# Kernel tuning notes

Measured on AMD Instinct MI355X. Metric: run time of the kernel, lower is better.

Reference implementation:

```python
import jax, jax.numpy as jnp
import numpy as np

E = 1024   # embed_dim
H = 16     # num_heads
D = E // H # head_dim
BS = 512   # block_size
G = 128    # global_len
B = 1
S = 8192


def setup_inputs() -> dict:
    key = jax.random.key(0)
    ks = jax.random.split(key, 7)
    w_scale = 0.02
    return {
        "token_hidden_states": jax.random.normal(ks[0], (B, S, E), jnp.float32),
        "global_hidden_states": jax.random.normal(ks[1], (B, G, E), jnp.float32),
        "attention_mask": jnp.zeros((B, S), jnp.float32),  # additive float mask
        "Wq": jax.random.normal(ks[2], (E, E), jnp.float32) * w_scale,
        "Wk": jax.random.normal(ks[3], (E, E), jnp.float32) * w_scale,
        "Wv": jax.random.normal(ks[4], (E, E), jnp.float32) * w_scale,
        "Wo": jax.random.normal(ks[5], (E, E), jnp.float32) * w_scale,
    }


def _shape(x):
    # [B, L, E] -> [B, H, L, D]
    b, l, _ = x.shape
    return x.reshape(b, l, H, D).transpose(0, 2, 1, 3)


def reference(token_hidden_states, global_hidden_states, attention_mask, Wq, Wk, Wv, Wo):
    b, s, _ = token_hidden_states.shape
    g = global_hidden_states.shape[1]
    n = s // BS  # num_blocks
    scaling = D ** -0.5

    local_q = _shape(token_hidden_states @ Wq * scaling)
    local_k = _shape(token_hidden_states @ Wk)
    local_v = _shape(token_hidden_states @ Wv)
    global_q = _shape(global_hidden_states @ Wq * scaling)
    global_k = _shape(global_hidden_states @ Wk)
    global_v = _shape(global_hidden_states @ Wv)

    # ---- global attention: global queries attend to [global + all local] keys
    k_cat = jnp.concatenate([global_k, local_k], axis=2)   # [B,H,G+S,D]
    v_cat = jnp.concatenate([global_v, local_v], axis=2)
    ext_mask = jnp.pad(attention_mask, ((0, 0), (g, 0)))    # [B,G+S]
    gw = jnp.einsum('bhgf,bhxf->bhgx', global_q, k_cat) + ext_mask[:, None, None, :]
    gp = jax.nn.softmax(gw, axis=-1)
    g_out = jnp.einsum('bhgx,bhxf->bhgf', gp, v_cat)        # [B,H,G,D]
    g_out = g_out.transpose(0, 2, 1, 3).reshape(b, g, E) @ Wo

    # ---- local attention: block-local + global keys
    bq = local_q.reshape(b, H, n, BS, D)
    bk = local_k.reshape(b, H, n, BS, D)
    bv = local_v.reshape(b, H, n, BS, D)
    ext_mask_l = jnp.pad(attention_mask.reshape(b, n, BS), ((0, 0), (0, 0), (g, 0)))  # [B,N,G+K]
    l2g = jnp.einsum('bhnkf,bhgf->bhnkg', bq, global_k)     # [B,H,N,K,G]
    l2l = jnp.einsum('bhnkf,bhnxf->bhnkx', bq, bk)          # [B,H,N,K,K]
    lw = jnp.concatenate([l2g, l2l], axis=-1) + ext_mask_l[:, None, :, None, :]
    lp = jax.nn.softmax(lw, axis=-1)
    l_out = (jnp.einsum('bhnkg,bhgf->bhnkf', lp[..., :g], global_v)
             + jnp.einsum('bhnkx,bhnxf->bhnkf', lp[..., g:], bv))  # [B,H,N,K,D]
    l_out = l_out.transpose(0, 2, 3, 1, 4).reshape(b, s, E) @ Wo

    return (l_out, g_out)
```

## Files before the change

### kernel.cpp

```cpp
#include <hip/hip_runtime.h>
#include <stdint.h>

#define S_LEN  8192
#define G_LEN  128
#define E_DIM  1024
#define H_NUM  16
#define BS_LEN 512
#define R_TOT  8320
#define KBLK   128
#define XBLK   1040
#define NSPL   10
#define SPLW   832

typedef _Float16 half8    __attribute__((ext_vector_type(8)));
typedef _Float16 half4    __attribute__((ext_vector_type(4)));
typedef float    floatx4  __attribute__((ext_vector_type(4)));
typedef float    floatx16 __attribute__((ext_vector_type(16)));

#define QSCALE 0.18033688011112042f

#define OFF_XP   0
#define OFF_AOP  0
#define OFF_WP   17039360
#define SZ_WP1   2097152
#define OFF_QP   25427968
#define OFF_KP   42467328
#define OFF_VP   59506688
#define OFF_FH   76546048
#define OFF_OG   76579328
#define OFF_LG   81822208

__device__ __forceinline__ floatx16 zero16() {
  floatx16 v;
#pragma unroll
  for (int i = 0; i < 16; ++i) v[i] = 0.0f;
  return v;
}
__device__ __forceinline__ floatx4 zero4() {
  floatx4 v;
#pragma unroll
  for (int i = 0; i < 4; ++i) v[i] = 0.0f;
  return v;
}

__device__ __forceinline__ void gl_lds16(const void* g, void* l) {
  __builtin_amdgcn_global_load_lds(
      (const __attribute__((address_space(1))) void*)g,
      (__attribute__((address_space(3))) void*)l, 16, 0, 0);
}

__device__ __forceinline__ int pk_f16x2(float a, float b) {
  return __builtin_bit_cast(int, __builtin_amdgcn_cvt_pkrtz(a, b));
}

__global__ __launch_bounds__(256) void prep_k(const float* __restrict__ tok,
                                              const float* __restrict__ glob,
                                              const float* __restrict__ Wq,
                                              const float* __restrict__ Wk,
                                              const float* __restrict__ Wv,
                                              const float* __restrict__ Wo,
                                              const float* __restrict__ mask,
                                              char* __restrict__ ws) {
  __shared__ __align__(16) _Float16 tile[64 * 132];
  const int bx  = blockIdx.x;
  const int tid = threadIdx.x;
  if (bx < 1040) {
    const int r0 = (bx >> 3) * 64;
    const int c0 = (bx & 7) * 128;
#pragma unroll
    for (int kk = 0; kk < 8; ++kk) {
      int f   = tid + kk * 256;
      int row = f >> 5;
      int c4  = (f & 31) * 4;
      int r   = r0 + row;
      const float* src = (r < G_LEN) ? glob + (size_t)r * E_DIM
                                     : tok + (size_t)(r - G_LEN) * E_DIM;
      float4 v = *(const float4*)&src[c0 + c4];
      half4 h;
      h[0] = (_Float16)v.x; h[1] = (_Float16)v.y; h[2] = (_Float16)v.z; h[3] = (_Float16)v.w;
      *(half4*)&tile[row * 132 + c4] = h;
    }
    __syncthreads();
    _Float16* Xp = (_Float16*)(ws + OFF_XP);
#pragma unroll
    for (int uu = 0; uu < 4; ++uu) {
      int u    = tid + uu * 256;
      int kb_l = u >> 6;
      int row  = u & 63;
      half4 a = *(const half4*)&tile[row * 132 + kb_l * 8];
      half4 b = *(const half4*)&tile[row * 132 + kb_l * 8 + 4];
      half8 o;
      o[0] = a[0]; o[1] = a[1]; o[2] = a[2]; o[3] = a[3];
      o[4] = b[0]; o[5] = b[1]; o[6] = b[2]; o[7] = b[3];
      int kb = (c0 >> 3) + kb_l;
      *(half8*)&Xp[((size_t)kb * R_TOT + r0 + row) * 8] = o;
    }
  } else {
    int t = (bx - 1040) * 256 + tid;
    const int NW = 4 * KBLK * 1024;
    if (t < NW) {
      int w   = t >> 17;
      int rem = t & 131071;
      int kb  = rem >> 10;
      int n   = rem & 1023;
      const float* W = (w == 0) ? Wq : (w == 1) ? Wk : (w == 2) ? Wv : Wo;
      half8 v;
#pragma unroll
      for (int j = 0; j < 8; ++j)
        v[j] = (_Float16)W[(size_t)(kb * 8 + j) * 1024 + n];
      *(half8*)(ws + OFF_WP + (size_t)w * SZ_WP1 + (size_t)(kb * 1024 + n) * 16) = v;
    } else {
      int t2 = t - NW;
      if (t2 < R_TOT) {
        _Float16* fh = (_Float16*)(ws + OFF_FH);
        float m = (t2 < G_LEN) ? 0.0f : mask[t2 - G_LEN];
        fh[t2] = (_Float16)__expf(m);
      }
    }
  }
}

__device__ __forceinline__ void gemm_tile(const _Float16* __restrict__ Ap,
                                          const _Float16* __restrict__ Bp,
                                          int m0, int n0, _Float16* lds,
                                          floatx4 acc[4][4]) {
  const int tid  = threadIdx.x;
  const int wave = tid >> 6;
  const int lane = tid & 63;
  const int quad = lane >> 4;
  const int l16  = lane & 15;
  _Float16* As = lds;
  _Float16* Bs = lds + 8 * 128 * 8;
  const int wm = (wave >> 1) * 64;
  const int wn = (wave & 1) * 64;
  for (int step = 0; step < 16; ++step) {
#pragma unroll
    for (int ui = 0; ui < 8; ++ui) {
      const int u   = wave * 8 + ui;
      const int isB = u >> 4;
      const int vv  = u & 15;
      const int kb  = vv >> 1;
      const int rh  = vv & 1;
      const _Float16* src =
          isB ? Bp + (size_t)((step * 8 + kb) * 1024 + n0 + rh * 64 + lane) * 8
              : Ap + (size_t)((step * 8 + kb) * R_TOT + m0 + rh * 64 + lane) * 8;
      _Float16* dst = (isB ? Bs : As) + (kb * 128 + rh * 64) * 8;
      gl_lds16(src, dst);
    }
    __syncthreads();
#pragma unroll
    for (int kk = 0; kk < 2; ++kk) {
      half8 af[4], bf[4];
#pragma unroll
      for (int mt = 0; mt < 4; ++mt)
        af[mt] = *(const half8*)(As + ((kk * 4 + quad) * 128 + wm + mt * 16 + l16) * 8);
#pragma unroll
      for (int nt = 0; nt < 4; ++nt)
        bf[nt] = *(const half8*)(Bs + ((kk * 4 + quad) * 128 + wn + nt * 16 + l16) * 8);
#pragma unroll
      for (int mt = 0; mt < 4; ++mt)
#pragma unroll
        for (int nt = 0; nt < 4; ++nt)
          acc[mt][nt] = __builtin_amdgcn_mfma_f32_16x16x32_f16(bf[nt], af[mt], acc[mt][nt], 0, 0, 0);
    }
    __syncthreads();
  }
}

__global__ __launch_bounds__(256) void qkv_gemm_k(char* __restrict__ ws) {
  __shared__ __align__(16) _Float16 lds[2 * 8 * 128 * 8];
  const int z  = blockIdx.x >> 3;
  const int n0 = (blockIdx.x & 7) * 128;
  const int m0 = blockIdx.y * 128;
  floatx4 acc[4][4];
#pragma unroll
  for (int a = 0; a < 4; ++a)
#pragma unroll
    for (int b = 0; b < 4; ++b) acc[a][b] = zero4();
  gemm_tile((const _Float16*)(ws + OFF_XP),
            (const _Float16*)(ws + OFF_WP + (size_t)z * SZ_WP1), m0, n0, lds, acc);

  const int lane = threadIdx.x & 63, wave = threadIdx.x >> 6;
  const int quad = lane >> 4, l16 = lane & 15;
  const int wm = (wave >> 1) * 64, wn = (wave & 1) * 64;
  if (z < 2) {
    _Float16* dst = (_Float16*)(ws + (z == 0 ? OFF_QP : OFF_KP));
    const float scale = (z == 0) ? QSCALE : 1.0f;
#pragma unroll
    for (int mt = 0; mt < 4; ++mt)
#pragma unroll
      for (int nt = 0; nt < 4; ++nt) {
        int m  = m0 + wm + mt * 16 + l16;
        int nb = n0 + wn + nt * 16 + quad * 4;
        half4 h;
#pragma unroll
        for (int r = 0; r < 4; ++r) h[r] = (_Float16)(acc[mt][nt][r] * scale);
        int db = (nb >> 6) * 8 + ((nb & 63) >> 3);
        *(half4*)&dst[((size_t)db * R_TOT + m) * 8 + (nb & 7)] = h;
      }
  } else {
    _Float16* dst = (_Float16*)(ws + OFF_VP);
    const _Float16* fh = (const _Float16*)(ws + OFF_FH);
#pragma unroll
    for (int mt = 0; mt < 4; ++mt) {
      int m = m0 + wm + mt * 16 + l16;
      float fhm = (float)fh[m];
#pragma unroll
      for (int nt = 0; nt < 4; ++nt) {
        int nl = n0 + wn + nt * 16 + quad * 4;
#pragma unroll
        for (int r = 0; r < 4; ++r) {
          int n = nl + r;
          dst[(((size_t)(n >> 6) * XBLK + (m >> 3)) * 64 + (n & 63)) * 8 + (m & 7)] =
              (_Float16)(acc[mt][nt][r] * fhm);
        }
      }
    }
  }
}

__device__ __forceinline__ void attn_chunks(const _Float16* __restrict__ Kph,
                                            const _Float16* __restrict__ Vph,
                                            const _Float16* __restrict__ fh,
                                            const half8 qa[4], int lane,
                                            int kbase0, int nch,
                                            floatx16& o0, floatx16& o1, floatx16& lacc) {
  const int  half_ = lane >> 5;
  const int  c     = lane & 31;
  const bool hb    = half_ != 0;
  half8 kf[4];
#pragma unroll
  for (int ks = 0; ks < 4; ++ks)
    kf[ks] = *(const half8*)&Kph[(size_t)((ks * 2 + half_) * R_TOT + kbase0 + c) * 8];
  for (int ci = 0; ci < nch; ++ci) {
    const int kb = kbase0 + ci * 32;
    const int xb = kb >> 3;
    half8 vA0 = *(const half8*)&Vph[(size_t)((xb + half_) * 64 + c) * 8];
    half8 vA1 = *(const half8*)&Vph[(size_t)((xb + 2 + half_) * 64 + c) * 8];
    half8 vB0 = *(const half8*)&Vph[(size_t)((xb + half_) * 64 + 32 + c) * 8];
    half8 vB1 = *(const half8*)&Vph[(size_t)((xb + 2 + half_) * 64 + 32 + c) * 8];
    half8 f0 = *(const half8*)&fh[kb + half_ * 8];
    half8 f1 = *(const half8*)&fh[kb + 16 + half_ * 8];
    floatx16 s = zero16();
#pragma unroll
    for (int ks = 0; ks < 4; ++ks)
      s = __builtin_amdgcn_mfma_f32_32x32x16_f16(kf[ks], qa[ks], s, 0, 0, 0);
    const int kbn = (ci + 1 < nch) ? kb + 32 : kbase0;
#pragma unroll
    for (int ks = 0; ks < 4; ++ks)
      kf[ks] = *(const half8*)&Kph[(size_t)((ks * 2 + half_) * R_TOT + kbn + c) * 8];
    int pk[8];
#pragma unroll
    for (int i = 0; i < 8; ++i) {
      float e0 = __builtin_amdgcn_exp2f(s[2 * i]);
      float e1 = __builtin_amdgcn_exp2f(s[2 * i + 1]);
      pk[i] = pk_f16x2(e0, e1);
    }
    int sw[8];
#pragma unroll
    for (int i = 0; i < 8; ++i) sw[i] = __shfl_xor(pk[i], 32);
    int4 bi0, bi1;
    bi0.x = hb ? sw[2] : pk[0];  bi0.y = hb ? sw[3] : pk[1];
    bi0.z = hb ? pk[2] : sw[0];  bi0.w = hb ? pk[3] : sw[1];
    bi1.x = hb ? sw[6] : pk[4];  bi1.y = hb ? sw[7] : pk[5];
    bi1.z = hb ? pk[6] : sw[4];  bi1.w = hb ? pk[7] : sw[5];
    half8 b0 = __builtin_bit_cast(half8, bi0);
    half8 b1 = __builtin_bit_cast(half8, bi1);
    lacc = __builtin_amdgcn_mfma_f32_32x32x16_f16(f0, b0, lacc, 0, 0, 0);
    lacc = __builtin_amdgcn_mfma_f32_32x32x16_f16(f1, b1, lacc, 0, 0, 0);
    o0 = __builtin_amdgcn_mfma_f32_32x32x16_f16(vA0, b0, o0, 0, 0, 0);
    o0 = __builtin_amdgcn_mfma_f32_32x32x16_f16(vA1, b1, o0, 0, 0, 0);
    o1 = __builtin_amdgcn_mfma_f32_32x32x16_f16(vB0, b0, o1, 0, 0, 0);
    o1 = __builtin_amdgcn_mfma_f32_32x32x16_f16(vB1, b1, o1, 0, 0, 0);
  }
}

__global__ __launch_bounds__(256) void attn_local_k(char* __restrict__ ws) {
  const int wave = threadIdx.x >> 6, lane = threadIdx.x & 63;
  const int bx = blockIdx.x;
  const int h = bx >> 6, blk = (bx >> 2) & 15, qg = bx & 3;
  const _Float16* fh = (const _Float16*)(ws + OFF_FH);
  const int half_ = lane >> 5, c = lane & 31;
  const int qbase = G_LEN + blk * BS_LEN + qg * 128 + wave * 32;
  const _Float16* Qph = (const _Float16*)(ws + OFF_QP) + (size_t)h * 8 * R_TOT * 8;
  const _Float16* Kph = (const _Float16*)(ws + OFF_KP) + (size_t)h * 8 * R_TOT * 8;
  const _Float16* Vph = (const _Float16*)(ws + OFF_VP) + (size_t)h * XBLK * 64 * 8;
  half8 qa[4];
#pragma unroll
  for (int ks = 0; ks < 4; ++ks)
    qa[ks] = *(const half8*)&Qph[(size_t)((ks * 2 + half_) * R_TOT + qbase + c) * 8];
  floatx16 o0 = zero16(), o1 = zero16(), l = zero16();
  attn_chunks(Kph, Vph, fh, qa, lane, 0, G_LEN / 32, o0, o1, l);
  attn_chunks(Kph, Vph, fh, qa, lane, G_LEN + blk * BS_LEN, BS_LEN / 32, o0, o1, l);
  _Float16* AOp = (_Float16*)(ws + OFF_AOP);
  const float inv = 1.0f / l[0];
  const int m = qbase + c;
#pragma unroll
  for (int g = 0; g < 4; ++g) {
    half4 ha, hc;
#pragma unroll
    for (int i = 0; i < 4; ++i) {
      ha[i] = (_Float16)(o0[4 * g + i] * inv);
      hc[i] = (_Float16)(o1[4 * g + i] * inv);
    }
    *(half4*)&AOp[((size_t)(h * 8 + g) * R_TOT + m) * 8 + 4 * half_] = ha;
    *(half4*)&AOp[((size_t)(h * 8 + 4 + g) * R_TOT + m) * 8 + 4 * half_] = hc;
  }
}

__global__ __launch_bounds__(256) void attn_glob_k(char* __restrict__ ws) {
  const int wave = threadIdx.x >> 6, lane = threadIdx.x & 63;
  const int spl = blockIdx.x % NSPL, h = blockIdx.x / NSPL;
  const _Float16* fh = (const _Float16*)(ws + OFF_FH);
  const int half_ = lane >> 5, c = lane & 31;
  const int qbase = wave * 32;
  const _Float16* Qph = (const _Float16*)(ws + OFF_QP) + (size_t)h * 8 * R_TOT * 8;
  const _Float16* Kph = (const _Float16*)(ws + OFF_KP) + (size_t)h * 8 * R_TOT * 8;
  const _Float16* Vph = (const _Float16*)(ws + OFF_VP) + (size_t)h * XBLK * 64 * 8;
  half8 qa[4];
#pragma unroll
  for (int ks = 0; ks < 4; ++ks)
    qa[ks] = *(const half8*)&Qph[(size_t)((ks * 2 + half_) * R_TOT + qbase + c) * 8];
  floatx16 o0 = zero16(), o1 = zero16(), l = zero16();
  attn_chunks(Kph, Vph, fh, qa, lane, spl * SPLW, SPLW / 32, o0, o1, l);
  float* Og = (float*)(ws + OFF_OG);
  float* Lg = (float*)(ws + OFF_LG);
  const int q = qbase + c;
#pragma unroll
  for (int g = 0; g < 4; ++g) {
    float4 fa, fb;
    fa.x = o0[4 * g]; fa.y = o0[4 * g + 1]; fa.z = o0[4 * g + 2]; fa.w = o0[4 * g + 3];
    fb.x = o1[4 * g]; fb.y = o1[4 * g + 1]; fb.z = o1[4 * g + 2]; fb.w = o1[4 * g + 3];
    *(float4*)&Og[((size_t)(spl * H_NUM + h) * 128 + q) * 64 + 8 * g + 4 * half_] = fa;
    *(float4*)&Og[((size_t)(spl * H_NUM + h) * 128 + q) * 64 + 32 + 8 * g + 4 * half_] = fb;
  }
  if (half_ == 0) Lg[(spl * H_NUM + h) * 128 + q] = l[0];
}

__global__ void combine_k(char* __restrict__ ws) {
  int idx = blockIdx.x * 256 + threadIdx.x;
  int h = idx >> 13, rem = idx & 8191, q = rem >> 6, d = rem & 63;
  const float* Og = (const float*)(ws + OFF_OG);
  const float* Lg = (const float*)(ws + OFF_LG);
  float o = 0.0f, l = 0.0f;
#pragma unroll
  for (int s = 0; s < NSPL; ++s) {
    o += Og[(size_t)((s * H_NUM + h) * 128 + q) * 64 + d];
    l += Lg[(s * H_NUM + h) * 128 + q];
  }
  int n = h * 64 + d;
  ((_Float16*)(ws + OFF_AOP))[((size_t)(n >> 3) * R_TOT + q) * 8 + (n & 7)] = (_Float16)(o / l);
}

__global__ __launch_bounds__(256) void out_gemm_k(char* __restrict__ ws, float* __restrict__ dout) {
  __shared__ __align__(16) _Float16 lds[2 * 8 * 128 * 8];
  const int m0 = blockIdx.y * 128;
  const int n0 = blockIdx.x * 128;
  floatx4 acc[4][4];
#pragma unroll
  for (int a = 0; a < 4; ++a)
#pragma unroll
    for (int b = 0; b < 4; ++b) acc[a][b] = zero4();
  gemm_tile((const _Float16*)(ws + OFF_AOP),
            (const _Float16*)(ws + OFF_WP + 3 * (size_t)SZ_WP1), m0, n0, lds, acc);
  const int lane = threadIdx.x & 63, wave = threadIdx.x >> 6;
  const int quad = lane >> 4, l16 = lane & 15;
  const int wm = (wave >> 1) * 64, wn = (wave & 1) * 64;
#pragma unroll
  for (int mt = 0; mt < 4; ++mt)
#pragma unroll
    for (int nt = 0; nt < 4; ++nt) {
      int m  = m0 + wm + mt * 16 + l16;
      int nb = n0 + wn + nt * 16 + quad * 4;
      float4 f4;
      f4.x = acc[mt][nt][0]; f4.y = acc[mt][nt][1];
      f4.z = acc[mt][nt][2]; f4.w = acc[mt][nt][3];
      float* p = (m < G_LEN) ? (dout + (size_t)S_LEN * E_DIM + (size_t)m * E_DIM + nb)
                             : (dout + (size_t)(m - G_LEN) * E_DIM + nb);
      *(float4*)p = f4;
    }
}

extern "C" void kernel_launch(void* const* d_in, const int* in_sizes, int n_in,
                              void* d_out, int out_size, void* d_ws, size_t ws_size,
                              hipStream_t stream) {
  const float* tok  = (const float*)d_in[0];
  const float* glob = (const float*)d_in[1];
  const float* mask = (const float*)d_in[2];
  const float* Wq   = (const float*)d_in[3];
  const float* Wk   = (const float*)d_in[4];
  const float* Wv   = (const float*)d_in[5];
  const float* Wo   = (const float*)d_in[6];
  char*  ws   = (char*)d_ws;
  float* dout = (float*)d_out;

  prep_k<<<dim3(1040 + 2081), dim3(256), 0, stream>>>(tok, glob, Wq, Wk, Wv, Wo, mask, ws);
  qkv_gemm_k<<<dim3(24, 65), dim3(256), 0, stream>>>(ws);
  attn_local_k<<<dim3(1024), dim3(256), 0, stream>>>(ws);
  attn_glob_k<<<dim3(NSPL * H_NUM), dim3(256), 0, stream>>>(ws);
  combine_k<<<dim3(512), dim3(256), 0, stream>>>(ws);
  out_gemm_k<<<dim3(8, 65), dim3(256), 0, stream>>>(ws, dout);
}
```

Measured before the change: 267.6 us.

## Merge local and global attention kernels and software-pipeline QK scores one chunk ahead

Fuses the local and global attention launches into a single grid, with the global split blocks placed first so they overlap with local blocks and one launch gap disappears. The local path now runs the 4 global chunks and 16 block chunks in one loop using a seam offset instead of two calls. The chunk loop computes the next chunk's QK scores before doing the current chunk's exp and PV MFMAs, which hides MFMA latency at the cost of extra live registers.

```diff
diff --git a/kernel.cpp b/kernel.cpp
--- a/kernel.cpp
+++ b/kernel.cpp
@@ -219,21 +219,33 @@
   }
 }
 
-__device__ __forceinline__ void attn_chunks(const _Float16* __restrict__ Kph,
-                                            const _Float16* __restrict__ Vph,
-                                            const _Float16* __restrict__ fh,
-                                            const half8 qa[4], int lane,
-                                            int kbase0, int nch,
-                                            floatx16& o0, floatx16& o1, floatx16& lacc) {
+__device__ __forceinline__ void attn_core(const _Float16* __restrict__ Kph,
+                                          const _Float16* __restrict__ Vph,
+                                          const _Float16* __restrict__ fh,
+                                          const half8 qa[4], int lane,
+                                          int off, int seam, int nch,
+                                          floatx16& o0, floatx16& o1, floatx16& lacc) {
   const int  half_ = lane >> 5;
   const int  c     = lane & 31;
   const bool hb    = half_ != 0;
+  auto kbof = [&](int ci) { return ci * 32 + ((ci >= seam) ? off : 0); };
+
   half8 kf[4];
+  const int kb0 = kbof(0);
 #pragma unroll
   for (int ks = 0; ks < 4; ++ks)
-    kf[ks] = *(const half8*)&Kph[(size_t)((ks * 2 + half_) * R_TOT + kbase0 + c) * 8];
+    kf[ks] = *(const half8*)&Kph[(size_t)((ks * 2 + half_) * R_TOT + kb0 + c) * 8];
+  floatx16 s = zero16();
+#pragma unroll
+  for (int ks = 0; ks < 4; ++ks)
+    s = __builtin_amdgcn_mfma_f32_32x32x16_f16(kf[ks], qa[ks], s, 0, 0, 0);
+  const int kb1 = kbof(nch > 1 ? 1 : 0);
+#pragma unroll
+  for (int ks = 0; ks < 4; ++ks)
+    kf[ks] = *(const half8*)&Kph[(size_t)((ks * 2 + half_) * R_TOT + kb1 + c) * 8];
+
   for (int ci = 0; ci < nch; ++ci) {
-    const int kb = kbase0 + ci * 32;
+    const int kb = kbof(ci);
     const int xb = kb >> 3;
     half8 vA0 = *(const half8*)&Vph[(size_t)((xb + half_) * 64 + c) * 8];
     half8 vA1 = *(const half8*)&Vph[(size_t)((xb + 2 + half_) * 64 + c) * 8];
@@ -241,11 +253,11 @@
     half8 vB1 = *(const half8*)&Vph[(size_t)((xb + 2 + half_) * 64 + 32 + c) * 8];
     half8 f0 = *(const half8*)&fh[kb + half_ * 8];
     half8 f1 = *(const half8*)&fh[kb + 16 + half_ * 8];
-    floatx16 s = zero16();
+    floatx16 sn = zero16();
 #pragma unroll
     for (int ks = 0; ks < 4; ++ks)
-      s = __builtin_amdgcn_mfma_f32_32x32x16_f16(kf[ks], qa[ks], s, 0, 0, 0);
-    const int kbn = (ci + 1 < nch) ? kb + 32 : kbase0;
+      sn = __builtin_amdgcn_mfma_f32_32x32x16_f16(kf[ks], qa[ks], sn, 0, 0, 0);
+    const int kbn = kbof(ci + 2 < nch ? ci + 2 : nch - 1);
 #pragma unroll
     for (int ks = 0; ks < 4; ++ks)
       kf[ks] = *(const half8*)&Kph[(size_t)((ks * 2 + half_) * R_TOT + kbn + c) * 8];
@@ -272,69 +284,67 @@
     o0 = __builtin_amdgcn_mfma_f32_32x32x16_f16(vA1, b1, o0, 0, 0, 0);
     o1 = __builtin_amdgcn_mfma_f32_32x32x16_f16(vB0, b0, o1, 0, 0, 0);
     o1 = __builtin_amdgcn_mfma_f32_32x32x16_f16(vB1, b1, o1, 0, 0, 0);
-  }
-}
-
-__global__ __launch_bounds__(256) void attn_local_k(char* __restrict__ ws) {
+    s = sn;
+  }
+}
+
+__global__ __launch_bounds__(256) void attn_k(char* __restrict__ ws) {
   const int wave = threadIdx.x >> 6, lane = threadIdx.x & 63;
   const int bx = blockIdx.x;
-  const int h = bx >> 6, blk = (bx >> 2) & 15, qg = bx & 3;
   const _Float16* fh = (const _Float16*)(ws + OFF_FH);
   const int half_ = lane >> 5, c = lane & 31;
-  const int qbase = G_LEN + blk * BS_LEN + qg * 128 + wave * 32;
-  const _Float16* Qph = (const _Float16*)(ws + OFF_QP) + (size_t)h * 8 * R_TOT * 8;
-  const _Float16* Kph = (const _Float16*)(ws + OFF_KP) + (size_t)h * 8 * R_TOT * 8;
-  const _Float16* Vph = (const _Float16*)(ws + OFF_VP) + (size_t)h * XBLK * 64 * 8;
-  half8 qa[4];
-#pragma unroll
-  for (int ks = 0; ks < 4; ++ks)
-    qa[ks] = *(const half8*)&Qph[(size_t)((ks * 2 + half_) * R_TOT + qbase + c) * 8];
-  floatx16 o0 = zero16(), o1 = zero16(), l = zero16();
-  attn_chunks(Kph, Vph, fh, qa, lane, 0, G_LEN / 32, o0, o1, l);
-  attn_chunks(Kph, Vph, fh, qa, lane, G_LEN + blk * BS_LEN, BS_LEN / 32, o0, o1, l);
-  _Float16* AOp = (_Float16*)(ws + OFF_AOP);
-  const float inv = 1.0f / l[0];
-  const int m = qbase + c;
-#pragma unroll
-  for (int g = 0; g < 4; ++g) {
-    half4 ha, hc;
-#pragma unroll
-    for (int i = 0; i < 4; ++i) {
-      ha[i] = (_Float16)(o0[4 * g + i] * inv);
-      hc[i] = (_Float16)(o1[4 * g + i] * inv);
-    }
-    *(half4*)&AOp[((size_t)(h * 8 + g) * R_TOT + m) * 8 + 4 * half_] = ha;
-    *(half4*)&AOp[((size_t)(h * 8 + 4 + g) * R_TOT + m) * 8 + 4 * half_] = hc;
-  }
-}
-
-__global__ __launch_bounds__(256) void attn_glob_k(char* __restrict__ ws) {
-  const int wave = threadIdx.x >> 6, lane = threadIdx.x & 63;
-  const int spl = blockIdx.x % NSPL, h = blockIdx.x / NSPL;
-  const _Float16* fh = (const _Float16*)(ws + OFF_FH);
-  const int half_ = lane >> 5, c = lane & 31;
-  const int qbase = wave * 32;
-  const _Float16* Qph = (const _Float16*)(ws + OFF_QP) + (size_t)h * 8 * R_TOT * 8;
-  const _Float16* Kph = (const _Float16*)(ws + OFF_KP) + (size_t)h * 8 * R_TOT * 8;
-  const _Float16* Vph = (const _Float16*)(ws + OFF_VP) + (size_t)h * XBLK * 64 * 8;
-  half8 qa[4];
-#pragma unroll
-  for (int ks = 0; ks < 4; ++ks)
-    qa[ks] = *(const half8*)&Qph[(size_t)((ks * 2 + half_) * R_TOT + qbase + c) * 8];
-  floatx16 o0 = zero16(), o1 = zero16(), l = zero16();
-  attn_chunks(Kph, Vph, fh, qa, lane, spl * SPLW, SPLW / 32, o0, o1, l);
-  float* Og = (float*)(ws + OFF_OG);
-  float* Lg = (float*)(ws + OFF_LG);
-  const int q = qbase + c;
-#pragma unroll
-  for (int g = 0; g < 4; ++g) {
-    float4 fa, fb;
-    fa.x = o0[4 * g]; fa.y = o0[4 * g + 1]; fa.z = o0[4 * g + 2]; fa.w = o0[4 * g + 3];
-    fb.x = o1[4 * g]; fb.y = o1[4 * g + 1]; fb.z = o1[4 * g + 2]; fb.w = o1[4 * g + 3];
-    *(float4*)&Og[((size_t)(spl * H_NUM + h) * 128 + q) * 64 + 8 * g + 4 * half_] = fa;
-    *(float4*)&Og[((size_t)(spl * H_NUM + h) * 128 + q) * 64 + 32 + 8 * g + 4 * half_] = fb;
-  }
-  if (half_ == 0) Lg[(spl * H_NUM + h) * 128 + q] = l[0];
+  if (bx < NSPL * H_NUM) {
+    const int h = bx / NSPL, spl = bx % NSPL;
+    const int qbase = wave * 32;
+    const _Float16* Qph = (const _Float16*)(ws + OFF_QP) + (size_t)h * 8 * R_TOT * 8;
+    const _Float16* Kph = (const _Float16*)(ws + OFF_KP) + (size_t)h * 8 * R_TOT * 8;
+    const _Float16* Vph = (const _Float16*)(ws + OFF_VP) + (size_t)h * XBLK * 64 * 8;
+    half8 qa[4];
+#pragma unroll
+    for (int ks = 0; ks < 4; ++ks)
+      qa[ks] = *(const half8*)&Qph[(size_t)((ks * 2 + half_) * R_TOT + qbase + c) * 8];
+    floatx16 o0 = zero16(), o1 = zero16(), l = zero16();
+    attn_core(Kph, Vph, fh, qa, lane, spl * SPLW, 0, SPLW / 32, o0, o1, l);
+    float* Og = (float*)(ws + OFF_OG);
+    float* Lg = (float*)(ws + OFF_LG);
+    const int q = qbase + c;
+#pragma unroll
+    for (int g = 0; g < 4; ++g) {
+      float4 fa, fb;
+      fa.x = o0[4 * g]; fa.y = o0[4 * g + 1]; fa.z = o0[4 * g + 2]; fa.w = o0[4 * g + 3];
+      fb.x = o1[4 * g]; fb.y = o1[4 * g + 1]; fb.z = o1[4 * g + 2]; fb.w = o1[4 * g + 3];
+      *(float4*)&Og[((size_t)(spl * H_NUM + h) * 128 + q) * 64 + 8 * g + 4 * half_] = fa;
+      *(float4*)&Og[((size_t)(spl * H_NUM + h) * 128 + q) * 64 + 32 + 8 * g + 4 * half_] = fb;
+    }
+    if (half_ == 0) Lg[(spl * H_NUM + h) * 128 + q] = l[0];
+  } else {
+    const int t = bx - NSPL * H_NUM;
+    const int h = t >> 6, blk = (t >> 2) & 15, qg = t & 3;
+    const int qbase = G_LEN + blk * BS_LEN + qg * 128 + wave * 32;
+    const _Float16* Qph = (const _Float16*)(ws + OFF_QP) + (size_t)h * 8 * R_TOT * 8;
+    const _Float16* Kph = (const _Float16*)(ws + OFF_KP) + (size_t)h * 8 * R_TOT * 8;
+    const _Float16* Vph = (const _Float16*)(ws + OFF_VP) + (size_t)h * XBLK * 64 * 8;
+    half8 qa[4];
+#pragma unroll
+    for (int ks = 0; ks < 4; ++ks)
+      qa[ks] = *(const half8*)&Qph[(size_t)((ks * 2 + half_) * R_TOT + qbase + c) * 8];
+    floatx16 o0 = zero16(), o1 = zero16(), l = zero16();
+    attn_core(Kph, Vph, fh, qa, lane, blk * BS_LEN, 4, 20, o0, o1, l);
+    _Float16* AOp = (_Float16*)(ws + OFF_AOP);
+    const float inv = 1.0f / l[0];
+    const int m = qbase + c;
+#pragma unroll
+    for (int g = 0; g < 4; ++g) {
+      half4 ha, hc;
+#pragma unroll
+      for (int i = 0; i < 4; ++i) {
+        ha[i] = (_Float16)(o0[4 * g + i] * inv);
+        hc[i] = (_Float16)(o1[4 * g + i] * inv);
+      }
+      *(half4*)&AOp[((size_t)(h * 8 + g) * R_TOT + m) * 8 + 4 * half_] = ha;
+      *(half4*)&AOp[((size_t)(h * 8 + 4 + g) * R_TOT + m) * 8 + 4 * half_] = hc;
+    }
+  }
 }
 
 __global__ void combine_k(char* __restrict__ ws) {
@@ -396,8 +406,7 @@
 
   prep_k<<<dim3(1040 + 2081), dim3(256), 0, stream>>>(tok, glob, Wq, Wk, Wv, Wo, mask, ws);
   qkv_gemm_k<<<dim3(24, 65), dim3(256), 0, stream>>>(ws);
-  attn_local_k<<<dim3(1024), dim3(256), 0, stream>>>(ws);
-  attn_glob_k<<<dim3(NSPL * H_NUM), dim3(256), 0, stream>>>(ws);
+  attn_k<<<dim3(NSPL * H_NUM + 1024), dim3(256), 0, stream>>>(ws);
   combine_k<<<dim3(512), dim3(256), 0, stream>>>(ws);
   out_gemm_k<<<dim3(8, 65), dim3(256), 0, stream>>>(ws, dout);
 }
```

Result: faster. 254.3 us (-5.0%).
